# Kernel tuning notes

Hardware: AMD Instinct MI355X
Metric: run time of the kernel (lower is better)

The kernel has to match this reference:

```python
import jax, jax.numpy as jnp
import numpy as np

E = 1024
H = 16
DFF = 4 * E
EPS = 1e-5


def layer_norm(x, scale, bias):
    mu = jnp.mean(x, axis=-1, keepdims=True)
    var = jnp.var(x, axis=-1, keepdims=True)
    return (x - mu) * jax.lax.rsqrt(var + EPS) * scale + bias


def setup_inputs() -> dict:
    key = jax.random.key(0)
    ks = jax.random.split(key, 12)
    N, L = 2, 2048
    x = jax.random.normal(ks[0], (N, L, E), dtype=jnp.float32)
    attn_mask = jax.random.randint(ks[1], (N, H, L, L), 0, 2) == 1
    s = 0.02
    return {
        "x": x,
        "attn_mask": attn_mask,
        "ln1_s": jnp.ones((E,), jnp.float32),
        "ln1_b": jnp.zeros((E,), jnp.float32),
        "Wqkv": jax.random.normal(ks[2], (E, 3 * E), jnp.float32) * s,
        "bqkv": jnp.zeros((3 * E,), jnp.float32),
        "Wo": jax.random.normal(ks[3], (E, E), jnp.float32) * s,
        "bo": jnp.zeros((E,), jnp.float32),
        "ln2_s": jnp.ones((E,), jnp.float32),
        "ln2_b": jnp.zeros((E,), jnp.float32),
        "lnf_s": jnp.ones((E,), jnp.float32),
        "lnf_b": jnp.zeros((E,), jnp.float32),
        "W1": jax.random.normal(ks[4], (E, DFF), jnp.float32) * s,
        "b1": jnp.zeros((DFF,), jnp.float32),
        "W2": jax.random.normal(ks[5], (DFF, E), jnp.float32) * s,
        "b2": jnp.zeros((E,), jnp.float32),
    }


def reference(x, attn_mask, ln1_s, ln1_b, Wqkv, bqkv, Wo, bo,
              ln2_s, ln2_b, lnf_s, lnf_b, W1, b1, W2, b2):
    N, L, _ = x.shape
    D = E // H
    # --- self attention (pre-norm) ---
    h = layer_norm(x, ln1_s, ln1_b)
    qkv = h @ Wqkv + bqkv                      # [N,L,3E]
    q, k, v = jnp.split(qkv, 3, axis=-1)
    q = q.reshape(N, L, H, D)
    k = k.reshape(N, L, H, D)
    v = v.reshape(N, L, H, D)
    a = jnp.einsum('nqhd,nkhd->nhqk', q, k) * (D ** -0.5)  # [N,H,L,L]
    a = jnp.where(attn_mask, -jnp.inf, a)
    a = jax.nn.softmax(a, axis=-1)
    o = jnp.einsum('nhqk,nkhd->nqhd', a, v).reshape(N, L, E)
    o = o @ Wo + bo
    x = x + o
    # --- feedforward (norm_2 then FF's internal LN) ---
    h = layer_norm(x, ln2_s, ln2_b)
    h = layer_norm(h, lnf_s, lnf_b)
    h = jax.nn.gelu(h @ W1 + b1, approximate=False) @ W2 + b2
    return x + h
```

## Files before the change

kernel.cpp:

```cpp
#include <hip/hip_runtime.h>
#include <math.h>

#define E_DIM 1024
#define H_HEADS 16
#define D_HEAD 64
#define DFF_DIM 4096
#define L_SEQ 2048
#define N_BATCH 2
#define T_TOK (N_BATCH * L_SEQ)
#define HT64 ((size_t)H_HEADS * T_TOK * 64)

typedef __attribute__((ext_vector_type(8))) __bf16 bf16x8;
typedef __attribute__((ext_vector_type(4))) float f32x4;

__device__ __forceinline__ unsigned short f2bf(float f) {
  union { float f; unsigned int u; } v; v.f = f;
  unsigned int r = v.u + 0x7fffu + ((v.u >> 16) & 1u);
  return (unsigned short)(r >> 16);
}

__device__ __forceinline__ void gl2lds16(const void* g, void* l) {
  __builtin_amdgcn_global_load_lds(
      (const __attribute__((address_space(1))) unsigned int*)g,
      (__attribute__((address_space(3))) unsigned int*)l, 16, 0, 0);
}

__device__ __forceinline__ void block_reduce2(float& a, float& b, float* sm, int tid) {
#pragma unroll
  for (int off = 32; off > 0; off >>= 1) {
    a += __shfl_down(a, off);
    b += __shfl_down(b, off);
  }
  int wid = tid >> 6;
  if ((tid & 63) == 0) { sm[wid * 2] = a; sm[wid * 2 + 1] = b; }
  __syncthreads();
  a = sm[0] + sm[2] + sm[4] + sm[6];
  b = sm[1] + sm[3] + sm[5] + sm[7];
}

__global__ __launch_bounds__(256) void prep_kernel(
    const float* __restrict__ Wqkv, const float* __restrict__ Wo,
    const float* __restrict__ W1, const float* __restrict__ W2,
    unsigned short* __restrict__ o0, unsigned short* __restrict__ o1,
    unsigned short* __restrict__ o2, unsigned short* __restrict__ o3,
    const float* __restrict__ x, const float* __restrict__ ln1_s,
    const float* __restrict__ ln1_b, unsigned short* __restrict__ h1) {
  int b = blockIdx.x;
  int tid = threadIdx.x;
  if (b >= 12288) {
    int row = b - 12288;
    __shared__ float sm[8];
    float4 v = ((const float4*)(x + (size_t)row * E_DIM))[tid];
    float sum = v.x + v.y + v.z + v.w;
    float sq = v.x * v.x + v.y * v.y + v.z * v.z + v.w * v.w;
    block_reduce2(sum, sq, sm, tid);
    float mu = sum * (1.0f / E_DIM);
    float rs = rsqrtf(sq * (1.0f / E_DIM) - mu * mu + 1e-5f);
    float4 sv = ((const float4*)ln1_s)[tid];
    float4 bv = ((const float4*)ln1_b)[tid];
    ushort4 o4;
    o4.x = f2bf((v.x - mu) * rs * sv.x + bv.x);
    o4.y = f2bf((v.y - mu) * rs * sv.y + bv.y);
    o4.z = f2bf((v.z - mu) * rs * sv.z + bv.z);
    o4.w = f2bf((v.w - mu) * rs * sv.w + bv.w);
    ((ushort4*)(h1 + (size_t)row * E_DIM))[tid] = o4;
    return;
  }
  const float* in; unsigned short* out; int K, N, tile;
  if (b < 3072)      { in = Wqkv; out = o0; K = 1024; N = 3072; tile = b; }
  else if (b < 4096) { in = Wo;   out = o1; K = 1024; N = 1024; tile = b - 3072; }
  else if (b < 8192) { in = W1;   out = o2; K = 1024; N = 4096; tile = b - 4096; }
  else               { in = W2;   out = o3; K = 4096; N = 1024; tile = b - 8192; }
  int ntx = N >> 5;
  int n0 = (tile % ntx) * 32, k0 = (tile / ntx) * 32;
  __shared__ float tilebuf[32][33];
  int tx = tid & 31, ty = tid >> 5;
#pragma unroll
  for (int i = 0; i < 32; i += 8)
    tilebuf[ty + i][tx] = in[(size_t)(k0 + ty + i) * N + n0 + tx];
  __syncthreads();
#pragma unroll
  for (int i = 0; i < 32; i += 8)
    out[(size_t)(n0 + ty + i) * K + k0 + tx] = f2bf(tilebuf[tx][ty + i]);
}

__global__ __launch_bounds__(256) void ln2_kernel(
    const float* __restrict__ x, const float* __restrict__ s2,
    const float* __restrict__ b2, const float* __restrict__ sf,
    const float* __restrict__ bf_, unsigned short* __restrict__ out,
    const float* __restrict__ b2ff, float* __restrict__ out_init) {
  int row = blockIdx.x, tid = threadIdx.x;
  __shared__ float sm[8];
  float4 v = ((const float4*)(x + (size_t)row * E_DIM))[tid];
  {
    float4 bb = ((const float4*)b2ff)[tid];
    float4 oi;
    oi.x = v.x + bb.x; oi.y = v.y + bb.y; oi.z = v.z + bb.z; oi.w = v.w + bb.w;
    ((float4*)(out_init + (size_t)row * E_DIM))[tid] = oi;
  }
  float sum = v.x + v.y + v.z + v.w;
  float sq = v.x * v.x + v.y * v.y + v.z * v.z + v.w * v.w;
  block_reduce2(sum, sq, sm, tid);
  float mu = sum * (1.0f / E_DIM);
  float rs = rsqrtf(sq * (1.0f / E_DIM) - mu * mu + 1e-5f);
  float4 s2v = ((const float4*)s2)[tid];
  float4 b2v = ((const float4*)b2)[tid];
  float y0 = (v.x - mu) * rs * s2v.x + b2v.x;
  float y1 = (v.y - mu) * rs * s2v.y + b2v.y;
  float y2 = (v.z - mu) * rs * s2v.z + b2v.z;
  float y3 = (v.w - mu) * rs * s2v.w + b2v.w;
  float sum2 = y0 + y1 + y2 + y3;
  float sq2 = y0 * y0 + y1 * y1 + y2 * y2 + y3 * y3;
  __syncthreads();
  block_reduce2(sum2, sq2, sm, tid);
  float mu2 = sum2 * (1.0f / E_DIM);
  float rs2 = rsqrtf(sq2 * (1.0f / E_DIM) - mu2 * mu2 + 1e-5f);
  float4 sfv = ((const float4*)sf)[tid];
  float4 bfv = ((const float4*)bf_)[tid];
  ushort4 o4;
  o4.x = f2bf((y0 - mu2) * rs2 * sfv.x + bfv.x);
  o4.y = f2bf((y1 - mu2) * rs2 * sfv.y + bfv.y);
  o4.z = f2bf((y2 - mu2) * rs2 * sfv.z + bfv.z);
  o4.w = f2bf((y3 - mu2) * rs2 * sfv.w + bfv.w);
  ((ushort4*)(out + (size_t)row * E_DIM))[tid] = o4;
}

__device__ __forceinline__ float gelu_exact(float v) {
  float z = v * 0.70710678118f;
  float az = fabsf(z);
  float t = 1.0f / (1.0f + 0.3275911f * az);
  float poly = ((((1.061405429f * t - 1.453152027f) * t + 1.421413741f) * t -
                 0.284496736f) * t + 0.254829592f) * t;
  float y = 1.0f - poly * __expf(-az * az);
  float er = (z < 0.0f) ? -y : y;
  return 0.5f * v * (1.0f + er);
}

template <int EPI>
__global__ __launch_bounds__(256) void gemm_bt(
    const unsigned short* __restrict__ A, const unsigned short* __restrict__ Bt,
    const float* __restrict__ bias, const float* __restrict__ resid,
    void* __restrict__ outp, int M, int N, int K) {
  __shared__ unsigned short As[128 * 32];
  __shared__ unsigned short Bs[128 * 32];
  int tid = threadIdx.x;
  int lane = tid & 63, wave = tid >> 6;
  int m0 = blockIdx.y * 128, n0 = blockIdx.x * 128;
  int wm = (wave & 1) * 64, wn = (wave >> 1) * 64;
  int lm = lane & 15, lq = lane >> 4;

  int r0 = tid >> 2, coff = (tid & 3) * 8;
  const unsigned short* Abase = A + (size_t)m0 * K;
  const unsigned short* Bbase = Bt + (size_t)n0 * K;
  unsigned short* lA0 = As + wave * 512;
  unsigned short* lA1 = As + 2048 + wave * 512;
  unsigned short* lB0 = Bs + wave * 512;
  unsigned short* lB1 = Bs + 2048 + wave * 512;

  int ks = K / gridDim.z;
  int kb = ks * blockIdx.z;

  f32x4 acc[4][4] = {};
  for (int k0 = kb; k0 < kb + ks; k0 += 32) {
    __syncthreads();
    gl2lds16(Abase + (size_t)r0 * K + k0 + coff, lA0);
    gl2lds16(Abase + (size_t)(r0 + 64) * K + k0 + coff, lA1);
    gl2lds16(Bbase + (size_t)r0 * K + k0 + coff, lB0);
    gl2lds16(Bbase + (size_t)(r0 + 64) * K + k0 + coff, lB1);
    __syncthreads();
    bf16x8 a[4], b[4];
#pragma unroll
    for (int i = 0; i < 4; i++)
      a[i] = *(const bf16x8*)(As + (wm + i * 16 + lm) * 32 + lq * 8);
#pragma unroll
    for (int j = 0; j < 4; j++)
      b[j] = *(const bf16x8*)(Bs + (wn + j * 16 + lm) * 32 + lq * 8);
#pragma unroll
    for (int i = 0; i < 4; i++)
#pragma unroll
      for (int j = 0; j < 4; j++)
        acc[i][j] = __builtin_amdgcn_mfma_f32_16x16x32_bf16(a[i], b[j], acc[i][j], 0, 0, 0);
  }
#pragma unroll
  for (int i = 0; i < 4; i++)
#pragma unroll
    for (int j = 0; j < 4; j++) {
      int row = m0 + wm + i * 16 + lq * 4;
      int col = n0 + wn + j * 16 + lm;
      float bcol = (EPI == 4) ? 0.0f : bias[col];
#pragma unroll
      for (int r = 0; r < 4; r++) {
        float v = acc[i][j][r] + bcol;
        if (EPI == 0) {
          ((unsigned short*)outp)[(size_t)(row + r) * N + col] = f2bf(v);
        } else if (EPI == 1) {
          ((unsigned short*)outp)[(size_t)(row + r) * N + col] = f2bf(gelu_exact(v));
        } else if (EPI == 2) {
          size_t idx = (size_t)(row + r) * N + col;
          ((float*)outp)[idx] = resid[idx] + v;
        } else if (EPI == 3) {
          int which = col >> 10, hh = (col & 1023) >> 6, d = col & 63;
          unsigned short* dst = (unsigned short*)outp + (size_t)which * HT64 +
                                ((size_t)hh * T_TOK + row + r) * 64 + d;
          *dst = f2bf(v);
        } else {
          atomicAdd((float*)outp + (size_t)(row + r) * N + col, v);
        }
      }
    }
}

__global__ __launch_bounds__(256) void attn_kernel(
    const unsigned short* __restrict__ qkvh, const int* __restrict__ mask,
    unsigned short* __restrict__ o, const float* __restrict__ x,
    const float* __restrict__ bo, float* __restrict__ x2) {
  const int bq = blockIdx.x;
  const int nh = blockIdx.y;
  const int h = nh & 15;
  const int tid = threadIdx.x, lane = tid & 63, wave = tid >> 6;
  const int lm = lane & 15, lq = lane >> 4;

  __shared__ unsigned short Ks[64 * 72];
  __shared__ unsigned short Vt[64 * 72];
  __shared__ unsigned short Ps[4][16 * 80];
  __shared__ unsigned int Msk[64 * 17];

  const int q_base = bq * 64;
  const int tok0 = (nh >> 4) * L_SEQ;
  const unsigned short* qh = qkvh + (size_t)h * T_TOK * 64;
  const unsigned short* kh = qkvh + HT64 + (size_t)h * T_TOK * 64;
  const unsigned short* vh = qkvh + 2 * HT64 + (size_t)h * T_TOK * 64;
  const int* mbase = mask + (size_t)nh * L_SEQ * L_SEQ;

  bf16x8 qf[2];
  {
    int t = tok0 + q_base + wave * 16 + lm;
    qf[0] = *(const bf16x8*)(qh + (size_t)t * 64 + lq * 8);
    qf[1] = *(const bf16x8*)(qh + (size_t)t * 64 + 32 + lq * 8);
  }

  const int skey = tid >> 3, schunk = tid & 7;
  const int mq0 = (tid >> 4) * 4, mkc = tid & 15;
  const int qrow = q_base + wave * 16 + lq * 4;
  const int* mcol = mbase + (size_t)(q_base + mq0) * L_SEQ + mkc * 4;

  float l_acc[4] = {0.0f, 0.0f, 0.0f, 0.0f};
  f32x4 oacc[4] = {};

  uint4 kv0, kv1, vv0, vv1;
  int4 mr0, mr1, mr2, mr3;
  {
    kv0 = *(const uint4*)(kh + (size_t)(tok0 + skey) * 64 + schunk * 8);
    kv1 = *(const uint4*)(kh + (size_t)(tok0 + skey + 32) * 64 + schunk * 8);
    vv0 = *(const uint4*)(vh + (size_t)(tok0 + skey) * 64 + schunk * 8);
    vv1 = *(const uint4*)(vh + (size_t)(tok0 + skey + 32) * 64 + schunk * 8);
    mr0 = *(const int4*)(mcol);
    mr1 = *(const int4*)(mcol + L_SEQ);
    mr2 = *(const int4*)(mcol + 2 * L_SEQ);
    mr3 = *(const int4*)(mcol + 3 * L_SEQ);
  }

  const float C1 = 0.125f * 1.44269504f;
  const float C2 = 12.0f * 1.44269504f;
  const int NT = L_SEQ / 64;
  for (int kt = 0; kt < NT; kt++) {
    __syncthreads();
    *(uint4*)(Ks + skey * 72 + schunk * 8) = kv0;
    *(uint4*)(Ks + (skey + 32) * 72 + schunk * 8) = kv1;
    {
      const unsigned short* p0 = (const unsigned short*)&vv0;
      const unsigned short* p1 = (const unsigned short*)&vv1;
#pragma unroll
      for (int jj = 0; jj < 8; jj++) {
        int jx = (jj + schunk) & 7;
        Vt[(schunk * 8 + jx) * 72 + skey] = p0[jx];
        Vt[(schunk * 8 + jx) * 72 + skey + 32] = p1[jx];
      }
    }
    {
      const int* a0 = (const int*)&mr0;
      const int* a1 = (const int*)&mr1;
      const int* a2 = (const int*)&mr2;
      const int* a3 = (const int*)&mr3;
#pragma unroll
      for (int kk = 0; kk < 4; kk++) {
        unsigned u = (a0[kk] ? 1u : 0u) | (a1[kk] ? 256u : 0u) |
                     (a2[kk] ? 65536u : 0u) | (a3[kk] ? 16777216u : 0u);
        Msk[(mkc * 4 + kk) * 17 + (mq0 >> 2)] = u;
      }
    }
    __syncthreads();

    if (kt + 1 < NT) {
      const int t1 = tok0 + (kt + 1) * 64;
      kv0 = *(const uint4*)(kh + (size_t)(t1 + skey) * 64 + schunk * 8);
      kv1 = *(const uint4*)(kh + (size_t)(t1 + skey + 32) * 64 + schunk * 8);
      vv0 = *(const uint4*)(vh + (size_t)(t1 + skey) * 64 + schunk * 8);
      vv1 = *(const uint4*)(vh + (size_t)(t1 + skey + 32) * 64 + schunk * 8);
      const int* mrow = mcol + (size_t)(kt + 1) * 64;
      mr0 = *(const int4*)(mrow);
      mr1 = *(const int4*)(mrow + L_SEQ);
      mr2 = *(const int4*)(mrow + 2 * L_SEQ);
      mr3 = *(const int4*)(mrow + 3 * L_SEQ);
    }

    f32x4 s[4];
#pragma unroll
    for (int nt = 0; nt < 4; nt++) {
      int key = nt * 16 + lm;
      bf16x8 kb0 = *(const bf16x8*)(Ks + key * 72 + lq * 8);
      bf16x8 kb1 = *(const bf16x8*)(Ks + key * 72 + 32 + lq * 8);
      f32x4 acc = {};
      acc = __builtin_amdgcn_mfma_f32_16x16x32_bf16(qf[0], kb0, acc, 0, 0, 0);
      acc = __builtin_amdgcn_mfma_f32_16x16x32_bf16(qf[1], kb1, acc, 0, 0, 0);
      s[nt] = acc;
    }
    unsigned short* pw = Ps[wave];
#pragma unroll
    for (int nt = 0; nt < 4; nt++) {
      unsigned mu = Msk[(nt * 16 + lm) * 17 + wave * 4 + lq];
#pragma unroll
      for (int r = 0; r < 4; r++) {
        float p = __builtin_amdgcn_exp2f(s[nt][r] * C1 - C2);
        p = ((mu >> (8 * r)) & 0xffu) ? 0.0f : p;
        l_acc[r] += p;
        pw[(lq * 4 + r) * 80 + nt * 16 + lm] = f2bf(p);
      }
    }
#pragma unroll
    for (int c = 0; c < 2; c++) {
      bf16x8 pa = *(const bf16x8*)(pw + lm * 80 + c * 32 + lq * 8);
#pragma unroll
      for (int j = 0; j < 4; j++) {
        bf16x8 vb = *(const bf16x8*)(Vt + (j * 16 + lm) * 72 + c * 32 + lq * 8);
        oacc[j] = __builtin_amdgcn_mfma_f32_16x16x32_bf16(pa, vb, oacc[j], 0, 0, 0);
      }
    }
  }
#pragma unroll
  for (int r = 0; r < 4; r++) {
#pragma unroll
    for (int mo = 1; mo < 16; mo <<= 1) l_acc[r] += __shfl_xor(l_acc[r], mo);
  }
#pragma unroll
  for (int r = 0; r < 4; r++) {
    float inv_l = 1.0f / l_acc[r];
    int t = tok0 + qrow + r;
#pragma unroll
    for (int j = 0; j < 4; j++) {
      int col = h * 64 + j * 16 + lm;
      o[(size_t)t * E_DIM + col] = f2bf(oacc[j][r] * inv_l);
      x2[(size_t)t * E_DIM + col] = x[(size_t)t * E_DIM + col] + bo[col];
    }
  }
}

extern "C" void kernel_launch(void* const* d_in, const int* in_sizes, int n_in,
                              void* d_out, int out_size, void* d_ws, size_t ws_size,
                              hipStream_t stream) {
  const float* x = (const float*)d_in[0];
  const int* mask = (const int*)d_in[1];
  const float* ln1_s = (const float*)d_in[2];
  const float* ln1_b = (const float*)d_in[3];
  const float* Wqkv = (const float*)d_in[4];
  const float* bqkv = (const float*)d_in[5];
  const float* Wo = (const float*)d_in[6];
  const float* bo = (const float*)d_in[7];
  const float* ln2_s = (const float*)d_in[8];
  const float* ln2_b = (const float*)d_in[9];
  const float* lnf_s = (const float*)d_in[10];
  const float* lnf_b = (const float*)d_in[11];
  const float* W1 = (const float*)d_in[12];
  const float* b1 = (const float*)d_in[13];
  const float* W2 = (const float*)d_in[14];
  const float* b2 = (const float*)d_in[15];

  size_t off = 0;
  auto alloc = [&](size_t bytes) {
    void* p = (char*)d_ws + off;
    off += (bytes + 255) & ~(size_t)255;
    return p;
  };
  unsigned short* WqkvT = (unsigned short*)alloc((size_t)3072 * 1024 * 2);
  unsigned short* WoT = (unsigned short*)alloc((size_t)1024 * 1024 * 2);
  unsigned short* W1T = (unsigned short*)alloc((size_t)4096 * 1024 * 2);
  unsigned short* W2T = (unsigned short*)alloc((size_t)1024 * 4096 * 2);
  unsigned short* h1 = (unsigned short*)alloc((size_t)T_TOK * E_DIM * 2);
  unsigned short* qkvh = (unsigned short*)alloc(3 * HT64 * 2);
  unsigned short* ob = (unsigned short*)alloc((size_t)T_TOK * E_DIM * 2);
  float* x2 = (float*)alloc((size_t)T_TOK * E_DIM * 4);
  unsigned short* h2 = (unsigned short*)alloc((size_t)T_TOK * E_DIM * 2);
  unsigned short* g1 = (unsigned short*)alloc((size_t)T_TOK * DFF_DIM * 2);

  prep_kernel<<<12288 + T_TOK, 256, 0, stream>>>(
      Wqkv, Wo, W1, W2, WqkvT, WoT, W1T, W2T, x, ln1_s, ln1_b, h1);
  gemm_bt<3><<<dim3(3072 / 128, T_TOK / 128), 256, 0, stream>>>(
      h1, WqkvT, bqkv, nullptr, qkvh, T_TOK, 3072, 1024);
  attn_kernel<<<dim3(L_SEQ / 64, N_BATCH * H_HEADS), 256, 0, stream>>>(
      qkvh, mask, ob, x, bo, x2);
  gemm_bt<4><<<dim3(1024 / 128, T_TOK / 128, 4), 256, 0, stream>>>(
      ob, WoT, nullptr, nullptr, x2, T_TOK, 1024, 1024);
  ln2_kernel<<<T_TOK, 256, 0, stream>>>(x2, ln2_s, ln2_b, lnf_s, lnf_b, h2,
                                        b2, (float*)d_out);
  gemm_bt<1><<<dim3(DFF_DIM / 128, T_TOK / 128), 256, 0, stream>>>(
      h2, W1T, b1, nullptr, g1, T_TOK, DFF_DIM, 1024);
  gemm_bt<4><<<dim3(1024 / 128, T_TOK / 128, 4), 256, 0, stream>>>(
      g1, W2T, nullptr, nullptr, (float*)d_out, T_TOK, 1024, 4096);

  (void)in_sizes; (void)n_in; (void)out_size; (void)ws_size;
}
```

Baseline: 1.227 ms.

## Store V transposed from QKV GEMM, swap QK MFMA operands, double-buffer mask loads

The QKV GEMM epilogue now writes V in a head-dim-major (transposed) layout, so the attention kernel can copy V tiles into LDS with vector stores instead of a per-element transpose. The QK^T MFMA operands are swapped so each lane holds scores for one query row. This lets the P tile be written as packed ushort4, the mask be laid out per query row, and the row sum be kept as a single scalar reduced with fewer shuffles. Mask loads are prefetched two tiles ahead, and the x+bo residual initialisation moves from the attention epilogue into the LayerNorm prep blocks. The transposed V stores in the GEMM epilogue are strided by T_TOK and may coalesce poorly, and the extra mask registers raise register pressure.

```diff
diff --git a/kernel.cpp b/kernel.cpp
--- a/kernel.cpp
+++ b/kernel.cpp
@@ -44,13 +44,20 @@
     unsigned short* __restrict__ o0, unsigned short* __restrict__ o1,
     unsigned short* __restrict__ o2, unsigned short* __restrict__ o3,
     const float* __restrict__ x, const float* __restrict__ ln1_s,
-    const float* __restrict__ ln1_b, unsigned short* __restrict__ h1) {
+    const float* __restrict__ ln1_b, unsigned short* __restrict__ h1,
+    const float* __restrict__ bo, float* __restrict__ x2) {
   int b = blockIdx.x;
   int tid = threadIdx.x;
   if (b >= 12288) {
     int row = b - 12288;
     __shared__ float sm[8];
     float4 v = ((const float4*)(x + (size_t)row * E_DIM))[tid];
+    {
+      float4 bb = ((const float4*)bo)[tid];
+      float4 oi;
+      oi.x = v.x + bb.x; oi.y = v.y + bb.y; oi.z = v.z + bb.z; oi.w = v.w + bb.w;
+      ((float4*)(x2 + (size_t)row * E_DIM))[tid] = oi;
+    }
     float sum = v.x + v.y + v.z + v.w;
     float sq = v.x * v.x + v.y * v.y + v.z * v.z + v.w * v.w;
     block_reduce2(sum, sq, sm, tid);
@@ -191,18 +198,16 @@
 #pragma unroll
       for (int r = 0; r < 4; r++) {
         float v = acc[i][j][r] + bcol;
-        if (EPI == 0) {
-          ((unsigned short*)outp)[(size_t)(row + r) * N + col] = f2bf(v);
-        } else if (EPI == 1) {
+        if (EPI == 1) {
           ((unsigned short*)outp)[(size_t)(row + r) * N + col] = f2bf(gelu_exact(v));
-        } else if (EPI == 2) {
-          size_t idx = (size_t)(row + r) * N + col;
-          ((float*)outp)[idx] = resid[idx] + v;
         } else if (EPI == 3) {
           int which = col >> 10, hh = (col & 1023) >> 6, d = col & 63;
-          unsigned short* dst = (unsigned short*)outp + (size_t)which * HT64 +
-                                ((size_t)hh * T_TOK + row + r) * 64 + d;
-          *dst = f2bf(v);
+          if (which == 2) {
+            ((unsigned short*)outp)[2 * HT64 + ((size_t)hh * 64 + d) * T_TOK + row + r] = f2bf(v);
+          } else {
+            ((unsigned short*)outp)[(size_t)which * HT64 +
+                                    ((size_t)hh * T_TOK + row + r) * 64 + d] = f2bf(v);
+          }
         } else {
           atomicAdd((float*)outp + (size_t)(row + r) * N + col, v);
         }
@@ -212,8 +217,7 @@
 
 __global__ __launch_bounds__(256) void attn_kernel(
     const unsigned short* __restrict__ qkvh, const int* __restrict__ mask,
-    unsigned short* __restrict__ o, const float* __restrict__ x,
-    const float* __restrict__ bo, float* __restrict__ x2) {
+    unsigned short* __restrict__ o) {
   const int bq = blockIdx.x;
   const int nh = blockIdx.y;
   const int h = nh & 15;
@@ -222,14 +226,14 @@
 
   __shared__ unsigned short Ks[64 * 72];
   __shared__ unsigned short Vt[64 * 72];
-  __shared__ unsigned short Ps[4][16 * 80];
+  __shared__ unsigned short Ps[4][16 * 72];
   __shared__ unsigned int Msk[64 * 17];
 
   const int q_base = bq * 64;
   const int tok0 = (nh >> 4) * L_SEQ;
   const unsigned short* qh = qkvh + (size_t)h * T_TOK * 64;
   const unsigned short* kh = qkvh + HT64 + (size_t)h * T_TOK * 64;
-  const unsigned short* vh = qkvh + 2 * HT64 + (size_t)h * T_TOK * 64;
+  const unsigned short* vt = qkvh + 2 * HT64 + (size_t)h * 64 * T_TOK;
   const int* mbase = mask + (size_t)nh * L_SEQ * L_SEQ;
 
   bf16x8 qf[2];
@@ -240,24 +244,29 @@
   }
 
   const int skey = tid >> 3, schunk = tid & 7;
+  const int vd = tid >> 3, vchunk = tid & 7;
   const int mq0 = (tid >> 4) * 4, mkc = tid & 15;
   const int qrow = q_base + wave * 16 + lq * 4;
   const int* mcol = mbase + (size_t)(q_base + mq0) * L_SEQ + mkc * 4;
 
-  float l_acc[4] = {0.0f, 0.0f, 0.0f, 0.0f};
+  float l_sum = 0.0f;
   f32x4 oacc[4] = {};
 
   uint4 kv0, kv1, vv0, vv1;
-  int4 mr0, mr1, mr2, mr3;
+  int4 ma0, ma1, ma2, ma3, mb0, mb1, mb2, mb3;
   {
     kv0 = *(const uint4*)(kh + (size_t)(tok0 + skey) * 64 + schunk * 8);
     kv1 = *(const uint4*)(kh + (size_t)(tok0 + skey + 32) * 64 + schunk * 8);
-    vv0 = *(const uint4*)(vh + (size_t)(tok0 + skey) * 64 + schunk * 8);
-    vv1 = *(const uint4*)(vh + (size_t)(tok0 + skey + 32) * 64 + schunk * 8);
-    mr0 = *(const int4*)(mcol);
-    mr1 = *(const int4*)(mcol + L_SEQ);
-    mr2 = *(const int4*)(mcol + 2 * L_SEQ);
-    mr3 = *(const int4*)(mcol + 3 * L_SEQ);
+    vv0 = *(const uint4*)(vt + (size_t)vd * T_TOK + tok0 + vchunk * 8);
+    vv1 = *(const uint4*)(vt + (size_t)(vd + 32) * T_TOK + tok0 + vchunk * 8);
+    ma0 = *(const int4*)(mcol);
+    ma1 = *(const int4*)(mcol + L_SEQ);
+    ma2 = *(const int4*)(mcol + 2 * L_SEQ);
+    ma3 = *(const int4*)(mcol + 3 * L_SEQ);
+    mb0 = *(const int4*)(mcol + 64);
+    mb1 = *(const int4*)(mcol + 64 + L_SEQ);
+    mb2 = *(const int4*)(mcol + 64 + 2 * L_SEQ);
+    mb3 = *(const int4*)(mcol + 64 + 3 * L_SEQ);
   }
 
   const float C1 = 0.125f * 1.44269504f;
@@ -267,27 +276,21 @@
     __syncthreads();
     *(uint4*)(Ks + skey * 72 + schunk * 8) = kv0;
     *(uint4*)(Ks + (skey + 32) * 72 + schunk * 8) = kv1;
+    *(uint4*)(Vt + vd * 72 + vchunk * 8) = vv0;
+    *(uint4*)(Vt + (vd + 32) * 72 + vchunk * 8) = vv1;
     {
-      const unsigned short* p0 = (const unsigned short*)&vv0;
-      const unsigned short* p1 = (const unsigned short*)&vv1;
-#pragma unroll
-      for (int jj = 0; jj < 8; jj++) {
-        int jx = (jj + schunk) & 7;
-        Vt[(schunk * 8 + jx) * 72 + skey] = p0[jx];
-        Vt[(schunk * 8 + jx) * 72 + skey + 32] = p1[jx];
-      }
-    }
-    {
-      const int* a0 = (const int*)&mr0;
-      const int* a1 = (const int*)&mr1;
-      const int* a2 = (const int*)&mr2;
-      const int* a3 = (const int*)&mr3;
-#pragma unroll
-      for (int kk = 0; kk < 4; kk++) {
-        unsigned u = (a0[kk] ? 1u : 0u) | (a1[kk] ? 256u : 0u) |
-                     (a2[kk] ? 65536u : 0u) | (a3[kk] ? 16777216u : 0u);
-        Msk[(mkc * 4 + kk) * 17 + (mq0 >> 2)] = u;
-      }
+      const int* a0 = (const int*)&ma0;
+      const int* a1 = (const int*)&ma1;
+      const int* a2 = (const int*)&ma2;
+      const int* a3 = (const int*)&ma3;
+      Msk[(mq0 + 0) * 17 + mkc] = (a0[0] ? 1u : 0u) | (a0[1] ? 256u : 0u) |
+                                  (a0[2] ? 65536u : 0u) | (a0[3] ? 16777216u : 0u);
+      Msk[(mq0 + 1) * 17 + mkc] = (a1[0] ? 1u : 0u) | (a1[1] ? 256u : 0u) |
+                                  (a1[2] ? 65536u : 0u) | (a1[3] ? 16777216u : 0u);
+      Msk[(mq0 + 2) * 17 + mkc] = (a2[0] ? 1u : 0u) | (a2[1] ? 256u : 0u) |
+                                  (a2[2] ? 65536u : 0u) | (a2[3] ? 16777216u : 0u);
+      Msk[(mq0 + 3) * 17 + mkc] = (a3[0] ? 1u : 0u) | (a3[1] ? 256u : 0u) |
+                                  (a3[2] ? 65536u : 0u) | (a3[3] ? 16777216u : 0u);
     }
     __syncthreads();
 
@@ -295,13 +298,16 @@
       const int t1 = tok0 + (kt + 1) * 64;
       kv0 = *(const uint4*)(kh + (size_t)(t1 + skey) * 64 + schunk * 8);
       kv1 = *(const uint4*)(kh + (size_t)(t1 + skey + 32) * 64 + schunk * 8);
-      vv0 = *(const uint4*)(vh + (size_t)(t1 + skey) * 64 + schunk * 8);
-      vv1 = *(const uint4*)(vh + (size_t)(t1 + skey + 32) * 64 + schunk * 8);
-      const int* mrow = mcol + (size_t)(kt + 1) * 64;
-      mr0 = *(const int4*)(mrow);
-      mr1 = *(const int4*)(mrow + L_SEQ);
-      mr2 = *(const int4*)(mrow + 2 * L_SEQ);
-      mr3 = *(const int4*)(mrow + 3 * L_SEQ);
+      vv0 = *(const uint4*)(vt + (size_t)vd * T_TOK + t1 + vchunk * 8);
+      vv1 = *(const uint4*)(vt + (size_t)(vd + 32) * T_TOK + t1 + vchunk * 8);
+    }
+    ma0 = mb0; ma1 = mb1; ma2 = mb2; ma3 = mb3;
+    if (kt + 2 < NT) {
+      const int* mrow = mcol + (size_t)(kt + 2) * 64;
+      mb0 = *(const int4*)(mrow);
+      mb1 = *(const int4*)(mrow + L_SEQ);
+      mb2 = *(const int4*)(mrow + 2 * L_SEQ);
+      mb3 = *(const int4*)(mrow + 3 * L_SEQ);
     }
 
     f32x4 s[4];
@@ -311,25 +317,27 @@
       bf16x8 kb0 = *(const bf16x8*)(Ks + key * 72 + lq * 8);
       bf16x8 kb1 = *(const bf16x8*)(Ks + key * 72 + 32 + lq * 8);
       f32x4 acc = {};
-      acc = __builtin_amdgcn_mfma_f32_16x16x32_bf16(qf[0], kb0, acc, 0, 0, 0);
-      acc = __builtin_amdgcn_mfma_f32_16x16x32_bf16(qf[1], kb1, acc, 0, 0, 0);
+      acc = __builtin_amdgcn_mfma_f32_16x16x32_bf16(kb0, qf[0], acc, 0, 0, 0);
+      acc = __builtin_amdgcn_mfma_f32_16x16x32_bf16(kb1, qf[1], acc, 0, 0, 0);
       s[nt] = acc;
     }
     unsigned short* pw = Ps[wave];
 #pragma unroll
     for (int nt = 0; nt < 4; nt++) {
-      unsigned mu = Msk[(nt * 16 + lm) * 17 + wave * 4 + lq];
+      unsigned mu = Msk[(wave * 16 + lm) * 17 + nt * 4 + lq];
+      ushort4 pk;
 #pragma unroll
       for (int r = 0; r < 4; r++) {
         float p = __builtin_amdgcn_exp2f(s[nt][r] * C1 - C2);
         p = ((mu >> (8 * r)) & 0xffu) ? 0.0f : p;
-        l_acc[r] += p;
-        pw[(lq * 4 + r) * 80 + nt * 16 + lm] = f2bf(p);
+        l_sum += p;
+        ((unsigned short*)&pk)[r] = f2bf(p);
       }
+      *(ushort4*)(pw + lm * 72 + nt * 16 + lq * 4) = pk;
     }
 #pragma unroll
     for (int c = 0; c < 2; c++) {
-      bf16x8 pa = *(const bf16x8*)(pw + lm * 80 + c * 32 + lq * 8);
+      bf16x8 pa = *(const bf16x8*)(pw + lm * 72 + c * 32 + lq * 8);
 #pragma unroll
       for (int j = 0; j < 4; j++) {
         bf16x8 vb = *(const bf16x8*)(Vt + (j * 16 + lm) * 72 + c * 32 + lq * 8);
@@ -337,21 +345,15 @@
       }
     }
   }
+  l_sum += __shfl_xor(l_sum, 16);
+  l_sum += __shfl_xor(l_sum, 32);
 #pragma unroll
   for (int r = 0; r < 4; r++) {
-#pragma unroll
-    for (int mo = 1; mo < 16; mo <<= 1) l_acc[r] += __shfl_xor(l_acc[r], mo);
-  }
-#pragma unroll
-  for (int r = 0; r < 4; r++) {
-    float inv_l = 1.0f / l_acc[r];
+    float inv_l = 1.0f / __shfl(l_sum, lq * 4 + r);
     int t = tok0 + qrow + r;
 #pragma unroll
-    for (int j = 0; j < 4; j++) {
-      int col = h * 64 + j * 16 + lm;
-      o[(size_t)t * E_DIM + col] = f2bf(oacc[j][r] * inv_l);
-      x2[(size_t)t * E_DIM + col] = x[(size_t)t * E_DIM + col] + bo[col];
-    }
+    for (int j = 0; j < 4; j++)
+      o[(size_t)t * E_DIM + h * 64 + j * 16 + lm] = f2bf(oacc[j][r] * inv_l);
   }
 }
 
@@ -393,11 +395,11 @@
   unsigned short* g1 = (unsigned short*)alloc((size_t)T_TOK * DFF_DIM * 2);
 
   prep_kernel<<<12288 + T_TOK, 256, 0, stream>>>(
-      Wqkv, Wo, W1, W2, WqkvT, WoT, W1T, W2T, x, ln1_s, ln1_b, h1);
+      Wqkv, Wo, W1, W2, WqkvT, WoT, W1T, W2T, x, ln1_s, ln1_b, h1, bo, x2);
   gemm_bt<3><<<dim3(3072 / 128, T_TOK / 128), 256, 0, stream>>>(
       h1, WqkvT, bqkv, nullptr, qkvh, T_TOK, 3072, 1024);
   attn_kernel<<<dim3(L_SEQ / 64, N_BATCH * H_HEADS), 256, 0, stream>>>(
-      qkvh, mask, ob, x, bo, x2);
+      qkvh, mask, ob);
   gemm_bt<4><<<dim3(1024 / 128, T_TOK / 128, 4), 256, 0, stream>>>(
       ob, WoT, nullptr, nullptr, x2, T_TOK, 1024, 1024);
   ln2_kernel<<<T_TOK, 256, 0, stream>>>(x2, ln2_s, ln2_b, lnf_s, lnf_b, h2,
```

New measurement: 1.074 ms. 12.5% less time.
